# Kernel tuning notes

Hardware: AMD Instinct MI355X
Metric: run time of the kernel (lower is better)

The kernel has to match this reference:

```python
import jax, jax.numpy as jnp
import numpy as np

B, S, D, L, E, C = 4, 512, 768, 10, 25, 9  # batch, seq, enc dim, max span len, len-embed dim, n labels


def _span_ids(seq_len, max_span_len):
    # replicates get_all_span_ids: distinct (start, min(start+k, seq_len)) for k in 1..max_span_len
    starts, ends = [], []
    for i in range(seq_len):
        seen = set()
        for k in range(1, max_span_len + 1):
            e = min(i + k, seq_len)
            if e not in seen:
                seen.add(e)
                starts.append(i)
                ends.append(e)
    return np.asarray(starts, np.int32), np.asarray(ends, np.int32)


def setup_inputs() -> dict:
    key = jax.random.key(0)
    k1, k2, k3 = jax.random.split(key, 3)
    st, en = _span_ids(S, L)  # N = 5075 spans
    return {
        "word_encodings": jax.random.normal(k1, (B, S, D), jnp.float32),
        "len_embed": jax.random.normal(k2, (L, E), jnp.float32) * 0.02,
        "W": jax.random.normal(k3, (D + E, C), jnp.float32) * 0.02,
        "b": jnp.zeros((C,), jnp.float32),
        "span_starts": jnp.asarray(st),
        "span_ends": jnp.asarray(en),
    }


def reference(word_encodings, len_embed, W, b, span_starts, span_ends):
    # word_encodings: [B,S,D]; span_starts/ends: [N] with end - start <= L
    N = span_starts.shape[0]
    pos = span_starts[:, None] + jnp.arange(L, dtype=span_starts.dtype)  # [N,L]
    valid = pos < span_ends[:, None]                                     # [N,L]
    pos_c = jnp.minimum(pos, S - 1)
    gathered = word_encodings[:, pos_c]                                  # [B,N,L,D]
    neg = jnp.asarray(-1e30, word_encodings.dtype)
    pooled = jnp.max(jnp.where(valid[None, :, :, None], gathered, neg), axis=2)  # [B,N,D]
    lens = span_ends - span_starts - 1                                   # [N] in [0, L)
    le = jnp.broadcast_to(len_embed[lens][None], (pooled.shape[0], N, E))  # [B,N,E]
    rep = jnp.concatenate([pooled, le], axis=-1)                         # [B,N,D+E]
    scores = jnp.einsum('bnf,fc->bnc', rep, W) + b                       # [B,N,C]
    return scores
```

## Files before the change

kernel.cpp:

```cpp
#include <hip/hip_runtime.h>


#define SS 512
#define DD 768
#define LL 10
#define EE 25
#define CC 9
#define NSPANS 5075

__device__ __forceinline__ float wave_sum64(float v) {
    int x;
    x = __builtin_amdgcn_update_dpp(0, __float_as_int(v), 0xB1, 0xF, 0xF, true);
    v += __int_as_float(x);
    x = __builtin_amdgcn_update_dpp(0, __float_as_int(v), 0x4E, 0xF, 0xF, true);
    v += __int_as_float(x);
    x = __builtin_amdgcn_update_dpp(0, __float_as_int(v), 0x141, 0xF, 0xF, true);
    v += __int_as_float(x);
    x = __builtin_amdgcn_update_dpp(0, __float_as_int(v), 0x140, 0xF, 0xF, true);
    v += __int_as_float(x);
    v += __shfl_xor(v, 16, 64);
    v += __shfl_xor(v, 32, 64);
    return v;
}

__global__ __launch_bounds__(256, 2) void spanner_kernel(
    const float* __restrict__ we,
    const float* __restrict__ lene,
    const float* __restrict__ W,
    const float* __restrict__ bias,
    float* __restrict__ out)
{
    __shared__ float lenW[LL][CC];
    const int t = threadIdx.x;

    if (t < LL * CC) {
        const int l = t / CC, c = t % CC;
        float s = bias[c];
#pragma unroll
        for (int e = 0; e < EE; ++e)
            s += lene[l * EE + e] * W[(DD + e) * CC + c];
        lenW[l][c] = s;
    }
    __syncthreads();

    const int lane = t & 63;
    const int gid  = blockIdx.x * 4 + (t >> 6);
    const int b    = gid >> 9;
    const int i    = gid & (SS - 1);
    const int cnt  = min(LL, SS - i);
    const int base = (i <= SS - LL) ? i * LL
                     : (NSPANS - ((SS - i) * (SS - i + 1)) / 2);

    float Wr[3][4][CC];
#pragma unroll
    for (int c0 = 0; c0 < 3; ++c0) {
        const float4* wp = reinterpret_cast<const float4*>(W + (c0 * 256 + lane * 4) * CC);
        float4 wv[9];
#pragma unroll
        for (int j = 0; j < 9; ++j) wv[j] = wp[j];
        const float* wf = reinterpret_cast<const float*>(wv);
#pragma unroll
        for (int q = 0; q < 4; ++q)
#pragma unroll
            for (int c = 0; c < CC; ++c)
                Wr[c0][q][c] = wf[q * CC + c];
    }

    const float4* rowbase = reinterpret_cast<const float4*>(we) + (size_t)(b * SS) * (DD / 4);

    float4 r0 = rowbase[(size_t)i * (DD / 4) + lane];
    float4 r1 = rowbase[(size_t)i * (DD / 4) + 64 + lane];
    float4 r2 = rowbase[(size_t)i * (DD / 4) + 128 + lane];

    float m[3][4];
#pragma unroll
    for (int c0 = 0; c0 < 3; ++c0)
#pragma unroll
        for (int q = 0; q < 4; ++q) m[c0][q] = -INFINITY;

    float acc[5][CC];
    float res[LL];

#pragma unroll
    for (int k = 0; k < LL; ++k) {
        {
            const float* f;
            f = (const float*)&r0;
#pragma unroll
            for (int q = 0; q < 4; ++q) m[0][q] = fmaxf(m[0][q], f[q]);
            f = (const float*)&r1;
#pragma unroll
            for (int q = 0; q < 4; ++q) m[1][q] = fmaxf(m[1][q], f[q]);
            f = (const float*)&r2;
#pragma unroll
            for (int q = 0; q < 4; ++q) m[2][q] = fmaxf(m[2][q], f[q]);
        }

        if (k + 1 < LL) {
            const int nr = min(i + k + 1, SS - 1);
            r0 = rowbase[(size_t)nr * (DD / 4) + lane];
            r1 = rowbase[(size_t)nr * (DD / 4) + 64 + lane];
            r2 = rowbase[(size_t)nr * (DD / 4) + 128 + lane];
        }

        const int kk = k % 5;
#pragma unroll
        for (int c = 0; c < CC; ++c) acc[kk][c] = 0.0f;
#pragma unroll
        for (int c0 = 0; c0 < 3; ++c0)
#pragma unroll
            for (int q = 0; q < 4; ++q)
#pragma unroll
                for (int c = 0; c < CC; ++c)
                    acc[kk][c] = fmaf(m[c0][q], Wr[c0][q][c], acc[kk][c]);

        if (kk == 4) {
#pragma unroll
            for (int kb = 0; kb < 5; ++kb) {
                float s[CC];
#pragma unroll
                for (int c = 0; c < CC; ++c) s[c] = wave_sum64(acc[kb][c]);
                float v = s[0];
#pragma unroll
                for (int c = 1; c < CC; ++c) v = (lane == c) ? s[c] : v;
                res[k - 4 + kb] = v;
            }
        }
    }

    float* const outb = out + ((size_t)b * NSPANS + base) * CC;
    if (lane < CC) {
#pragma unroll
        for (int k = 0; k < LL; ++k)
            if (k < cnt) outb[k * CC + lane] = res[k] + lenW[k][lane];
    }
}

extern "C" void kernel_launch(void* const* d_in, const int* in_sizes, int n_in,
                              void* d_out, int out_size, void* d_ws, size_t ws_size,
                              hipStream_t stream) {
    const float* we   = (const float*)d_in[0];
    const float* lene = (const float*)d_in[1];
    const float* W    = (const float*)d_in[2];
    const float* bias = (const float*)d_in[3];
    float* out        = (float*)d_out;

    spanner_kernel<<<512, 256, 0, stream>>>(we, lene, W, bias, out);
}
```

Measured before the change: 79.56 us.

## Split each span start across three waves with shared-memory partial reduction

```diff
diff --git a/kernel.cpp b/kernel.cpp
--- a/kernel.cpp
+++ b/kernel.cpp
@@ -7,8 +7,9 @@
 #define EE 25
 #define CC 9
 #define NSPANS 5075
+#define TPB 192
 
-__device__ __forceinline__ float wave_sum64(float v) {
+__device__ __forceinline__ float dpp_reduce16(float v) {
     int x;
     x = __builtin_amdgcn_update_dpp(0, __float_as_int(v), 0xB1, 0xF, 0xF, true);
     v += __int_as_float(x);
@@ -18,20 +19,28 @@
     v += __int_as_float(x);
     x = __builtin_amdgcn_update_dpp(0, __float_as_int(v), 0x140, 0xF, 0xF, true);
     v += __int_as_float(x);
-    v += __shfl_xor(v, 16, 64);
-    v += __shfl_xor(v, 32, 64);
     return v;
 }
 
-__global__ __launch_bounds__(256, 2) void spanner_kernel(
+__global__ __launch_bounds__(TPB, 4) void spanner_kernel(
     const float* __restrict__ we,
     const float* __restrict__ lene,
     const float* __restrict__ W,
     const float* __restrict__ bias,
     float* __restrict__ out)
 {
+    __shared__ __align__(16) float sp[LL][CC][3][4];
     __shared__ float lenW[LL][CC];
-    const int t = threadIdx.x;
+
+    const int t    = threadIdx.x;
+    const int lane = t & 63;
+    const int wvid = t >> 6;
+    const int gid  = blockIdx.x;
+    const int b    = gid >> 9;
+    const int i    = gid & (SS - 1);
+    const int cnt  = min(LL, SS - i);
+    const int base = (i <= SS - LL) ? i * LL
+                     : (NSPANS - ((SS - i) * (SS - i + 1)) / 2);
 
     if (t < LL * CC) {
         const int l = t / CC, c = t % CC;
@@ -41,98 +50,70 @@
             s += lene[l * EE + e] * W[(DD + e) * CC + c];
         lenW[l][c] = s;
     }
-    __syncthreads();
 
-    const int lane = t & 63;
-    const int gid  = blockIdx.x * 4 + (t >> 6);
-    const int b    = gid >> 9;
-    const int i    = gid & (SS - 1);
-    const int cnt  = min(LL, SS - i);
-    const int base = (i <= SS - LL) ? i * LL
-                     : (NSPANS - ((SS - i) * (SS - i + 1)) / 2);
-
-    float Wr[3][4][CC];
+    float Wr[4][CC];
+    {
+        const float4* wp = reinterpret_cast<const float4*>(W) + t * 9;
+        float4 wv4[9];
 #pragma unroll
-    for (int c0 = 0; c0 < 3; ++c0) {
-        const float4* wp = reinterpret_cast<const float4*>(W + (c0 * 256 + lane * 4) * CC);
-        float4 wv[9];
-#pragma unroll
-        for (int j = 0; j < 9; ++j) wv[j] = wp[j];
-        const float* wf = reinterpret_cast<const float*>(wv);
+        for (int j = 0; j < 9; ++j) wv4[j] = wp[j];
+        const float* wf = reinterpret_cast<const float*>(wv4);
 #pragma unroll
         for (int q = 0; q < 4; ++q)
 #pragma unroll
             for (int c = 0; c < CC; ++c)
-                Wr[c0][q][c] = wf[q * CC + c];
+                Wr[q][c] = wf[q * CC + c];
     }
 
-    const float4* rowbase = reinterpret_cast<const float4*>(we) + (size_t)(b * SS) * (DD / 4);
+    const float* rowb = we + ((size_t)b * SS) * DD + t * 4;
+    float4 r = *reinterpret_cast<const float4*>(rowb + (size_t)i * DD);
 
-    float4 r0 = rowbase[(size_t)i * (DD / 4) + lane];
-    float4 r1 = rowbase[(size_t)i * (DD / 4) + 64 + lane];
-    float4 r2 = rowbase[(size_t)i * (DD / 4) + 128 + lane];
+    float m[4] = {-INFINITY, -INFINITY, -INFINITY, -INFINITY};
 
-    float m[3][4];
-#pragma unroll
-    for (int c0 = 0; c0 < 3; ++c0)
-#pragma unroll
-        for (int q = 0; q < 4; ++q) m[c0][q] = -INFINITY;
-
-    float acc[5][CC];
-    float res[LL];
+    const int cs  = lane & 15;
+    const int grp = lane >> 4;
 
 #pragma unroll
-    for (int k = 0; k < LL; ++k) {
-        {
-            const float* f;
-            f = (const float*)&r0;
-#pragma unroll
-            for (int q = 0; q < 4; ++q) m[0][q] = fmaxf(m[0][q], f[q]);
-            f = (const float*)&r1;
-#pragma unroll
-            for (int q = 0; q < 4; ++q) m[1][q] = fmaxf(m[1][q], f[q]);
-            f = (const float*)&r2;
-#pragma unroll
-            for (int q = 0; q < 4; ++q) m[2][q] = fmaxf(m[2][q], f[q]);
+    for (int s = 0; s < LL; ++s) {
+        m[0] = fmaxf(m[0], r.x);
+        m[1] = fmaxf(m[1], r.y);
+        m[2] = fmaxf(m[2], r.z);
+        m[3] = fmaxf(m[3], r.w);
+
+        if (s + 1 < LL) {
+            const int nr = min(i + s + 1, SS - 1);
+            r = *reinterpret_cast<const float4*>(rowb + (size_t)nr * DD);
         }
 
-        if (k + 1 < LL) {
-            const int nr = min(i + k + 1, SS - 1);
-            r0 = rowbase[(size_t)nr * (DD / 4) + lane];
-            r1 = rowbase[(size_t)nr * (DD / 4) + 64 + lane];
-            r2 = rowbase[(size_t)nr * (DD / 4) + 128 + lane];
-        }
+        float acc[CC];
+#pragma unroll
+        for (int c = 0; c < CC; ++c) acc[c] = 0.0f;
+#pragma unroll
+        for (int q = 0; q < 4; ++q)
+#pragma unroll
+            for (int c = 0; c < CC; ++c)
+                acc[c] = fmaf(m[q], Wr[q][c], acc[c]);
 
-        const int kk = k % 5;
 #pragma unroll
-        for (int c = 0; c < CC; ++c) acc[kk][c] = 0.0f;
+        for (int c = 0; c < CC; ++c) acc[c] = dpp_reduce16(acc[c]);
+
+        float v = acc[0];
 #pragma unroll
-        for (int c0 = 0; c0 < 3; ++c0)
-#pragma unroll
-            for (int q = 0; q < 4; ++q)
-#pragma unroll
-                for (int c = 0; c < CC; ++c)
-                    acc[kk][c] = fmaf(m[c0][q], Wr[c0][q][c], acc[kk][c]);
-
-        if (kk == 4) {
-#pragma unroll
-            for (int kb = 0; kb < 5; ++kb) {
-                float s[CC];
-#pragma unroll
-                for (int c = 0; c < CC; ++c) s[c] = wave_sum64(acc[kb][c]);
-                float v = s[0];
-#pragma unroll
-                for (int c = 1; c < CC; ++c) v = (lane == c) ? s[c] : v;
-                res[k - 4 + kb] = v;
-            }
-        }
+        for (int c = 1; c < CC; ++c) v = (cs == c) ? acc[c] : v;
+        if (cs < CC) sp[s][cs][wvid][grp] = v;
     }
 
-    float* const outb = out + ((size_t)b * NSPANS + base) * CC;
-    if (lane < CC) {
-#pragma unroll
-        for (int k = 0; k < LL; ++k)
-            if (k < cnt) outb[k * CC + lane] = res[k] + lenW[k][lane];
+    __syncthreads();
+
+    if (t < LL * CC) {
+        const int s = t / CC, c = t % CC;
+        const float4* pp = reinterpret_cast<const float4*>(&sp[s][c][0][0]);
+        const float4 p0 = pp[0], p1 = pp[1], p2 = pp[2];
+        const float sum = ((p0.x + p0.y) + (p0.z + p0.w))
+                        + ((p1.x + p1.y) + (p1.z + p1.w))
+                        + ((p2.x + p2.y) + (p2.z + p2.w));
+        if (s < cnt)
+            out[((size_t)b * NSPANS + base + s) * CC + c] = sum + lenW[s][c];
     }
 }
 
@@ -145,5 +126,5 @@
     const float* bias = (const float*)d_in[3];
     float* out        = (float*)d_out;
 
-    spanner_kernel<<<512, 256, 0, stream>>>(we, lene, W, bias, out);
+    spanner_kernel<<<2048, TPB, 0, stream>>>(we, lene, W, bias, out);
 }
```

Measured after the change: 81.33 us. +2.2%, slower.
